# Performance work log

Measured on AMD Instinct MI355X. Metric: run time of the kernel, lower is better.

## Reference

```python
import jax, jax.numpy as jnp
from jax import lax
import numpy as np

B, N, T = 16, 1024, 12
H_DIM, D_FF, NHEADS = 64, 256, 4
SDIM, DDIM, WDIM = 32, 16, 15
D_IN = 1 + SDIM + DDIM + WDIM  # 64


def setup_inputs() -> dict:
    key = jax.random.key(0)
    ks = jax.random.split(key, 32)
    def p(k, shape, s=0.05):
        return jax.random.normal(k, shape, dtype=jnp.float32) * s
    h = H_DIM
    inp = {
        'flow': jax.random.normal(ks[0], (B, N, T), dtype=jnp.float32),
        'day_idx': jax.random.randint(ks[1], (B, N, T), 0, 288),
        'week_idx': jax.random.randint(ks[2], (B, N, T), 0, 7),
        'spatial_emb': p(ks[3], (N, SDIM)),
        'daily_emb': p(ks[4], (288, DDIM)),
        'weekly_emb': p(ks[5], (7, WDIM)),
        'gfs_fc_w': p(ks[6], (h, D_IN)), 'gfs_fc_b': jnp.zeros(h),
        'glu_w': p(ks[7], (2 * h, h)), 'glu_b': jnp.zeros(2 * h),
        'gc_weight': p(ks[8], (h, h)),
        'gc_A': p(ks[9], (N, N), 0.02), 'gc_A2': p(ks[10], (N, N), 0.02),
        'ds_init_w': p(ks[11], (2 * h, h, 1, 3)), 'ds_init_b': jnp.zeros(2 * h),
        'ds_p1m_w': p(ks[12], (h, h, 1, 3)), 'ds_p1m_b': jnp.zeros(h),
        'ds_p1g_w': p(ks[13], (h, h, 1, 3)), 'ds_p1g_b': jnp.zeros(h),
        'ds_p2m_w': p(ks[14], (h, h, 1, 3)), 'ds_p2m_b': jnp.zeros(h),
        'ds_p2g_w': p(ks[15], (h, h, 1, 3)), 'ds_p2g_b': jnp.zeros(h),
        'ds_fc_w': p(ks[16], (h, 2 * h)), 'ds_fc_b': jnp.zeros(h),
        'wq': p(ks[17], (h, h)), 'bq': jnp.zeros(h),
        'wk': p(ks[18], (h, h)), 'bk': jnp.zeros(h),
        'wv': p(ks[19], (h, h)), 'bv': jnp.zeros(h),
        'wo': p(ks[20], (h, h)), 'bo': jnp.zeros(h),
        'ff1_w': p(ks[21], (D_FF, h)), 'ff1_b': jnp.zeros(D_FF),
        'ff2_w': p(ks[22], (h, D_FF)), 'ff2_b': jnp.zeros(h),
        'ln1_g': jnp.ones(h), 'ln1_b': jnp.zeros(h),
        'ln2_g': jnp.ones(h), 'ln2_b': jnp.zeros(h),
        'cl_w': p(ks[23], (T,)), 'cl_b': jnp.zeros(()),
    }
    return inp


def _ln(x, g, b):
    m = jnp.mean(x, -1, keepdims=True)
    v = jnp.mean(jnp.square(x - m), -1, keepdims=True)
    return (x - m) * lax.rsqrt(v + 1e-5) * g + b


def _conv1xk(x, w, b):
    # x: [B, C, N, T], w: [O, I, 1, 3], padding (0,1) along time
    y = lax.conv_general_dilated(x, w, (1, 1), ((0, 0), (1, 1)),
                                 dimension_numbers=('NCHW', 'OIHW', 'NCHW'))
    return y + b[None, :, None, None]


def reference(flow, day_idx, week_idx, spatial_emb, daily_emb, weekly_emb,
              gfs_fc_w, gfs_fc_b, glu_w, glu_b, gc_weight, gc_A, gc_A2,
              ds_init_w, ds_init_b, ds_p1m_w, ds_p1m_b, ds_p1g_w, ds_p1g_b,
              ds_p2m_w, ds_p2m_b, ds_p2g_w, ds_p2g_b, ds_fc_w, ds_fc_b,
              wq, bq, wk, bk, wv, bv, wo, bo, ff1_w, ff1_b, ff2_w, ff2_b,
              ln1_g, ln1_b, ln2_g, ln2_b, cl_w, cl_b):
    h = H_DIM
    # --- InfoEmb: concat flow + spatial + daily + weekly embeddings ---
    sp = jnp.broadcast_to(spatial_emb[None, :, None, :], (B, N, T, SDIM))
    x = jnp.concatenate([flow[..., None], sp, daily_emb[day_idx], weekly_emb[week_idx]], -1)  # [B,N,T,64]
    # --- GFS: 1x1 conv + GLU (channels == last dim) ---
    x = x @ gfs_fc_w.T + gfs_fc_b
    g = x @ glu_w.T + glu_b
    lhs, rhs = g[..., :h], g[..., h:]
    x = lhs * jax.nn.sigmoid(rhs)  # [B,N,T,h]
    # --- TASTGC: adaptive spatial graph conv with two learned adjacencies ---
    A1 = jax.nn.softmax(jax.nn.relu(gc_A), axis=1)
    A2 = jax.nn.softmax(jax.nn.relu(gc_A2), axis=1)
    hs = jnp.einsum('mn,bntd->bmtd', A1, x) + jnp.einsum('mn,bntd->bmtd', A2, x)
    x = jax.nn.relu(jnp.einsum('bntd,de->bnte', hs, gc_weight))  # [B,N,T,h]
    # --- DSFIN: dual-path gated temporal conv ---
    xd = jnp.transpose(x, (0, 3, 1, 2))  # [B,h,N,T]
    x_init = _conv1xk(xd, ds_init_w, ds_init_b)  # [B,2h,N,T]
    p1, p2 = x_init[:, :h], x_init[:, h:]
    p1o = _conv1xk(p1, ds_p1m_w, ds_p1m_b) * jax.nn.sigmoid(_conv1xk(p1, ds_p1g_w, ds_p1g_b))
    p2o = _conv1xk(p2, ds_p2m_w, ds_p2m_b) * jax.nn.sigmoid(_conv1xk(p2, ds_p2g_w, ds_p2g_b))
    fused = jax.nn.relu(jnp.concatenate([p1o, p2o], 1) + x_init)  # [B,2h,N,T]
    fused = jnp.transpose(fused, (0, 2, 3, 1))  # [B,N,T,2h]
    x = fused @ ds_fc_w.T + ds_fc_b  # [B,N,T,h]
    # --- EncoderLayer: multi-head attention along time per node ---
    dk = h // NHEADS
    y = x.reshape(B * N, T, h)
    q = (y @ wq.T + bq).reshape(B * N, T, NHEADS, dk)
    k = (y @ wk.T + bk).reshape(B * N, T, NHEADS, dk)
    v = (y @ wv.T + bv).reshape(B * N, T, NHEADS, dk)
    scores = jnp.einsum('blhd,bshd->bhls', q, k) / jnp.sqrt(jnp.float32(dk))
    attn = jax.nn.softmax(scores, -1)
    o = jnp.einsum('bhls,bshd->blhd', attn, v).reshape(B * N, T, h)
    y1 = _ln(y + (o @ wo.T + bo), ln1_g, ln1_b)
    ff = jax.nn.relu(y1 @ ff1_w.T + ff1_b) @ ff2_w.T + ff2_b
    y2 = _ln(y1 + ff, ln2_g, ln2_b).reshape(B, N, T, h)
    # --- CongestionLearn: symmetric sigmoid node-node gate from flow ---
    f = jax.nn.relu(flow @ cl_w + cl_b)  # [B,N]
    m = jnp.mean(f, 0)  # [N]
    fuse = jax.nn.sigmoid((m[:, None] + m[None, :]) * 0.5)  # [N,N]
    out = jnp.einsum('mn,bntd->bmtd', fuse, y2)  # [B,N,T,h]
    return out
```

## Files before the change

kernel.cpp:

```cpp
#include <hip/hip_runtime.h>
#include <cstdint>

#define B_ 16
#define N_ 1024
#define T_ 12
#define HD 64
#define BN_ (B_*N_)
#define BNT (B_*N_*T_)
#define TD (T_*HD)

typedef __attribute__((ext_vector_type(8))) short short8;
typedef __attribute__((ext_vector_type(4))) float f32x4;

#define MFMA16(a,b,c) __builtin_amdgcn_mfma_f32_16x16x32_bf16(a,b,c,0,0,0)

__device__ __forceinline__ float sigmoidf_(float x) { return 1.f / (1.f + __expf(-x)); }

__device__ __forceinline__ unsigned short f2bf(float f) {
  unsigned int u = __float_as_uint(f);
  u += 0x7fffu + ((u >> 16) & 1u);
  return (unsigned short)(u >> 16);
}
__device__ __forceinline__ float bf2f(unsigned short h) {
  unsigned int u = ((unsigned int)h) << 16;
  return __uint_as_float(u);
}

#define F4E(v, ii) ((ii)==0?(v).x:((ii)==1?(v).y:((ii)==2?(v).z:(v).w)))

__device__ __forceinline__ float blkRedMax(float v, float* red) {
  #pragma unroll
  for (int off = 32; off >= 1; off >>= 1) v = fmaxf(v, __shfl_xor(v, off));
  int w = threadIdx.x >> 6;
  if ((threadIdx.x & 63) == 0) red[w] = v;
  __syncthreads();
  v = fmaxf(fmaxf(red[0], red[1]), fmaxf(red[2], red[3]));
  __syncthreads();
  return v;
}
__device__ __forceinline__ float blkRedSum(float v, float* red) {
  #pragma unroll
  for (int off = 32; off >= 1; off >>= 1) v += __shfl_xor(v, off);
  int w = threadIdx.x >> 6;
  if ((threadIdx.x & 63) == 0) red[w] = v;
  __syncthreads();
  v = red[0] + red[1] + red[2] + red[3];
  __syncthreads();
  return v;
}

__global__ void k_wprep_e(const float* __restrict__ w1, const float* __restrict__ w2,
                          float* __restrict__ wT)
{
  int tid = blockIdx.x*256 + threadIdx.x;
  if (tid < 4096) { int d = tid >> 6, j = tid & 63; wT[j*64 + d] = w1[tid]; }
  if (tid < 8192) { int o = tid >> 6, j = tid & 63; wT[4096 + j*128 + o] = w2[tid]; }
}

__global__ void k_wprep3(const float* __restrict__ wi,
                         const float* __restrict__ w1m, const float* __restrict__ w1g,
                         const float* __restrict__ w2m, const float* __restrict__ w2g,
                         const float* __restrict__ wfc, unsigned short* __restrict__ W)
{
  int t = blockIdx.x*256 + threadIdx.x;
  {
    int o = t / 192, k = t - o*192, tap = k >> 6, i = k & 63;
    W[o*192 + k] = f2bf(wi[(o*64 + i)*3 + tap]);
  }
  if (t < 12288) {
    int o = t / 192, k = t - o*192, tap = k >> 6, i = k & 63;
    int src = (o*64 + i)*3 + tap;
    W[24576 + o*192 + k]      = f2bf(w1m[src]);
    W[24576 + (64+o)*192 + k] = f2bf(w1g[src]);
    W[49152 + o*192 + k]      = f2bf(w2m[src]);
    W[49152 + (64+o)*192 + k] = f2bf(w2g[src]);
  }
  if (t < 8192) W[73728 + t] = f2bf(wfc[t]);
}

__global__ void k_wprep4(const float* __restrict__ wq, const float* __restrict__ wk,
                         const float* __restrict__ wv, const float* __restrict__ wo,
                         const float* __restrict__ f1w, const float* __restrict__ f2w,
                         unsigned short* __restrict__ W)
{
  int t = blockIdx.x*256 + threadIdx.x;
  if (t < 4096)        W[t] = f2bf(wq[t]);
  else if (t < 8192)   W[t] = f2bf(wk[t-4096]);
  else if (t < 12288)  W[t] = f2bf(wv[t-8192]);
  else if (t < 16384)  W[t] = f2bf(wo[t-12288]);
  else if (t < 32768)  W[t] = f2bf(f1w[t-16384]);
  else                 W[t] = f2bf(f2w[t-32768]);
}

__global__ __launch_bounds__(256) void k_embed2(
    const float* __restrict__ flow, const int* __restrict__ day, const int* __restrict__ week,
    const float* __restrict__ semb, const float* __restrict__ demb, const float* __restrict__ wemb,
    const float* __restrict__ wT, const float* __restrict__ b1,
    const float* __restrict__ b2, const float* __restrict__ gcw,
    unsigned short* __restrict__ outw)
{
  __shared__ float4 vb_all[4][256];
  int lane = threadIdx.x & 63, wid = threadIdx.x >> 6;
  float4* vb = vb_all[wid];
  const float* w1T = wT;
  const float* w2T = wT + 4096;
  int row0 = (blockIdx.x*4 + wid) * 16;

  float x[16];
  #pragma unroll
  for (int r = 0; r < 16; ++r) {
    int row = row0 + r;
    int n = (row / T_) & (N_-1);
    int c = lane;
    float val;
    if (c == 0)      val = flow[row];
    else if (c < 33) val = semb[n*32 + (c-1)];
    else if (c < 49) val = demb[day[row]*16 + (c-33)];
    else             val = wemb[week[row]*15 + (c-49)];
    x[r] = val;
  }
  #pragma unroll
  for (int q = 0; q < 4; ++q)
    vb[lane*4 + q] = make_float4(x[4*q], x[4*q+1], x[4*q+2], x[4*q+3]);

  float acc[16];
  {
    float bv = b1[lane];
    #pragma unroll
    for (int r = 0; r < 16; ++r) acc[r] = bv;
    for (int j = 0; j < 64; ++j) {
      float w = w1T[j*64 + lane];
      #pragma unroll
      for (int q = 0; q < 4; ++q) {
        float4 v = vb[j*4 + q];
        acc[4*q]   += w*v.x; acc[4*q+1] += w*v.y;
        acc[4*q+2] += w*v.z; acc[4*q+3] += w*v.w;
      }
    }
  }
  #pragma unroll
  for (int q = 0; q < 4; ++q)
    vb[lane*4 + q] = make_float4(acc[4*q], acc[4*q+1], acc[4*q+2], acc[4*q+3]);

  float lo[16], hi[16];
  {
    float blo = b2[lane], bhi = b2[64 + lane];
    #pragma unroll
    for (int r = 0; r < 16; ++r) { lo[r] = blo; hi[r] = bhi; }
    for (int j = 0; j < 64; ++j) {
      float wl = w2T[j*128 + lane];
      float wh = w2T[j*128 + 64 + lane];
      #pragma unroll
      for (int q = 0; q < 4; ++q) {
        float4 v = vb[j*4 + q];
        lo[4*q]   += wl*v.x; lo[4*q+1] += wl*v.y; lo[4*q+2] += wl*v.z; lo[4*q+3] += wl*v.w;
        hi[4*q]   += wh*v.x; hi[4*q+1] += wh*v.y; hi[4*q+2] += wh*v.z; hi[4*q+3] += wh*v.w;
      }
    }
    #pragma unroll
    for (int r = 0; r < 16; ++r) lo[r] = lo[r] * sigmoidf_(hi[r]);
  }
  #pragma unroll
  for (int q = 0; q < 4; ++q)
    vb[lane*4 + q] = make_float4(lo[4*q], lo[4*q+1], lo[4*q+2], lo[4*q+3]);

  {
    #pragma unroll
    for (int r = 0; r < 16; ++r) acc[r] = 0.f;
    for (int j = 0; j < 64; ++j) {
      float w = gcw[j*64 + lane];
      #pragma unroll
      for (int q = 0; q < 4; ++q) {
        float4 v = vb[j*4 + q];
        acc[4*q]   += w*v.x; acc[4*q+1] += w*v.y;
        acc[4*q+2] += w*v.z; acc[4*q+3] += w*v.w;
      }
    }
    #pragma unroll
    for (int r = 0; r < 16; ++r)
      outw[(size_t)(row0 + r)*64 + lane] = f2bf(acc[r]);
  }
}

__global__ __launch_bounds__(256) void k_aprep(
    const float* __restrict__ A1, const float* __restrict__ A2, unsigned short* __restrict__ Aout)
{
  __shared__ float red[4];
  int m = blockIdx.x, tid = threadIdx.x;
  float mx0, is0, mx1, is1;
  {
    const float* src = A1 + (size_t)m*N_;
    float mx = 0.f;
    for (int i = tid; i < N_; i += 256) mx = fmaxf(mx, fmaxf(src[i], 0.f));
    mx = blkRedMax(mx, red);
    float s = 0.f;
    for (int i = tid; i < N_; i += 256) s += __expf(fmaxf(src[i], 0.f) - mx);
    s = blkRedSum(s, red);
    mx0 = mx; is0 = 1.f / s;
  }
  {
    const float* src = A2 + (size_t)m*N_;
    float mx = 0.f;
    for (int i = tid; i < N_; i += 256) mx = fmaxf(mx, fmaxf(src[i], 0.f));
    mx = blkRedMax(mx, red);
    float s = 0.f;
    for (int i = tid; i < N_; i += 256) s += __expf(fmaxf(src[i], 0.f) - mx);
    s = blkRedSum(s, red);
    mx1 = mx; is1 = 1.f / s;
  }
  const float* s1 = A1 + (size_t)m*N_;
  const float* s2 = A2 + (size_t)m*N_;
  for (int i = tid; i < N_; i += 256) {
    float v1 = __expf(fmaxf(s1[i], 0.f) - mx0) * is0;
    float v2 = __expf(fmaxf(s2[i], 0.f) - mx1) * is1;
    Aout[(size_t)m*N_ + i] = f2bf(v1 + v2);
  }
}

template<int RELU, int OB16>
__global__ __launch_bounds__(256) void k_gemm_mfma(
    const unsigned short* __restrict__ A, const unsigned short* __restrict__ X,
    void* __restrict__ C, int K, int P)
{
  __shared__ unsigned short sA[128*40];
  __shared__ unsigned short sB[128*40];
  int tid = threadIdx.x, lane = tid & 63, wid = tid >> 6;
  int M = gridDim.y * 128;
  int b = blockIdx.z;
  const unsigned short* Xb = X + (size_t)b*K*P;
  int m0 = blockIdx.y*128, p0 = blockIdx.x*128;
  int wr = wid >> 1, wc = wid & 1;

  f32x4 acc[4][4] = {};

  for (int k0 = 0; k0 < K; k0 += 32) {
    #pragma unroll
    for (int pass = 0; pass < 2; ++pass) {
      int r = (tid >> 2) + 64*pass, kk = (tid & 3)*8;
      short8 v = *(const short8*)&A[(size_t)(m0+r)*K + k0 + kk];
      *(short8*)&sA[r*40 + kk] = v;
    }
    #pragma unroll
    for (int pass = 0; pass < 4; ++pass) {
      int p  = (tid & 63) + 64*(pass & 1);
      int k4 = (tid >> 6)*4 + 16*(pass >> 1);
      ushort4 h;
      h.x = Xb[(size_t)(k0+k4+0)*P + p0 + p];
      h.y = Xb[(size_t)(k0+k4+1)*P + p0 + p];
      h.z = Xb[(size_t)(k0+k4+2)*P + p0 + p];
      h.w = Xb[(size_t)(k0+k4+3)*P + p0 + p];
      *(ushort4*)&sB[p*40 + k4] = h;
    }
    __syncthreads();
    short8 af[4], bf[4];
    #pragma unroll
    for (int f = 0; f < 4; ++f) {
      af[f] = *(const short8*)&sA[(wr*64 + f*16 + (lane & 15))*40 + (lane >> 4)*8];
      bf[f] = *(const short8*)&sB[(wc*64 + f*16 + (lane & 15))*40 + (lane >> 4)*8];
    }
    #pragma unroll
    for (int fm = 0; fm < 4; ++fm)
      #pragma unroll
      for (int fn = 0; fn < 4; ++fn)
        acc[fm][fn] = MFMA16(af[fm], bf[fn], acc[fm][fn]);
    __syncthreads();
  }
  #pragma unroll
  for (int fm = 0; fm < 4; ++fm) {
    int row = m0 + wr*64 + fm*16 + (lane >> 4)*4;
    #pragma unroll
    for (int fn = 0; fn < 4; ++fn) {
      int col = p0 + wc*64 + fn*16 + (lane & 15);
      #pragma unroll
      for (int r = 0; r < 4; ++r) {
        float v = acc[fm][fn][r];
        if (RELU) v = fmaxf(v, 0.f);
        if (OB16) {
          unsigned short* Cb = (unsigned short*)C + (size_t)b*M*P;
          Cb[(size_t)(row + r)*P + col] = f2bf(v);
        } else {
          float* Cb = (float*)C + (size_t)b*M*P;
          Cb[(size_t)(row + r)*P + col] = v;
        }
      }
    }
  }
}

__global__ __launch_bounds__(256) void k_ds3(
    const unsigned short* xds,
    const unsigned short* __restrict__ Wall,
    const float* __restrict__ bi,
    const float* __restrict__ b1m, const float* __restrict__ b1g,
    const float* __restrict__ b2m, const float* __restrict__ b2g,
    const float* __restrict__ bfc,
    unsigned short* outg)
{
  __shared__ unsigned short smem[36352];
  unsigned short* X_lds  = smem;
  unsigned short* xi_lds = smem + 8064;
  unsigned short* fu_lds = smem + 23296;
  const unsigned short* WiB  = Wall;
  const unsigned short* Wg1B = Wall + 24576;
  const unsigned short* Wg2B = Wall + 49152;
  const unsigned short* WfB  = Wall + 73728;

  int tid = threadIdx.x, lane = tid & 63, wid = tid >> 6;
  int l15 = lane & 15, l4 = lane >> 4;
  int bn0 = blockIdx.x * 8;

  for (int i = tid; i < 8*2*72; i += 256) {
    int g = i / 144, r = i - g*144;
    int tp = (r < 72) ? 0 : 13, c = (r < 72) ? r : r - 72;
    X_lds[(g*14 + tp)*72 + c] = 0;
  }
  for (int i = tid; i < 8*2*136; i += 256) {
    int g = i / 272, r = i - g*272;
    int tp = (r < 136) ? 0 : 13, c = (r < 136) ? r : r - 136;
    xi_lds[(g*14 + tp)*136 + c] = 0;
  }
  for (int i = tid; i < 768; i += 256) {
    int g = i / 96, rem = i - g*96, t = rem >> 3, i8 = rem & 7;
    short8 v = *(const short8*)&xds[(size_t)(bn0+g)*768 + t*64 + i8*8];
    *(short8*)&X_lds[(g*14 + t + 1)*72 + i8*8] = v;
  }
  __syncthreads();

  int ga[6], ta[6];
  #pragma unroll
  for (int mt = 0; mt < 6; ++mt) {
    int r = mt*16 + l15;
    ga[mt] = r / 12; ta[mt] = r - ga[mt]*12;
  }

  {
    f32x4 acc1[6][2] = {};
    int nb = wid*2;
    #pragma unroll
    for (int ks = 0; ks < 6; ++ks) {
      int tap = ks >> 1, i0 = (ks & 1)*32;
      short8 af[6];
      #pragma unroll
      for (int mt = 0; mt < 6; ++mt)
        af[mt] = *(const short8*)&X_lds[(ga[mt]*14 + ta[mt] + tap)*72 + i0 + l4*8];
      short8 bf0 = *(const short8*)&WiB[(size_t)((nb  )*16 + l15)*192 + ks*32 + l4*8];
      short8 bf1 = *(const short8*)&WiB[(size_t)((nb+1)*16 + l15)*192 + ks*32 + l4*8];
      #pragma unroll
      for (int mt = 0; mt < 6; ++mt) {
        acc1[mt][0] = MFMA16(af[mt], bf0, acc1[mt][0]);
        acc1[mt][1] = MFMA16(af[mt], bf1, acc1[mt][1]);
      }
    }
    #pragma unroll
    for (int nn = 0; nn < 2; ++nn) {
      int o = (nb+nn)*16 + l15;
      float bv = bi[o];
      #pragma unroll
      for (int mt = 0; mt < 6; ++mt) {
        #pragma unroll
        for (int reg = 0; reg < 4; ++reg) {
          int r = mt*16 + l4*4 + reg;
          int g = r / 12, t = r - g*12;
          xi_lds[(g*14 + t + 1)*136 + o] = f2bf(acc1[mt][nn][reg] + bv);
        }
      }
    }
  }
  __syncthreads();

  #pragma unroll
  for (int h = 0; h < 2; ++h) {
    const unsigned short* Wg = h ? Wg2B : Wg1B;
    f32x4 am[6] = {}, ag[6] = {};
    #pragma unroll
    for (int ks = 0; ks < 6; ++ks) {
      int tap = ks >> 1, i0 = (ks & 1)*32;
      short8 af[6];
      #pragma unroll
      for (int mt = 0; mt < 6; ++mt)
        af[mt] = *(const short8*)&xi_lds[(ga[mt]*14 + ta[mt] + tap)*136 + h*64 + i0 + l4*8];
      short8 bm = *(const short8*)&Wg[(size_t)(wid*16 + l15)*192 + ks*32 + l4*8];
      short8 bg = *(const short8*)&Wg[(size_t)((wid+4)*16 + l15)*192 + ks*32 + l4*8];
      #pragma unroll
      for (int mt = 0; mt < 6; ++mt) {
        am[mt] = MFMA16(af[mt], bm, am[mt]);
        ag[mt] = MFMA16(af[mt], bg, ag[mt]);
      }
    }
    int o = wid*16 + l15;
    float bmv = (h ? b2m : b1m)[o];
    float bgv = (h ? b2g : b1g)[o];
    #pragma unroll
    for (int mt = 0; mt < 6; ++mt) {
      #pragma unroll
      for (int reg = 0; reg < 4; ++reg) {
        int r = mt*16 + l4*4 + reg;
        int g = r / 12, t = r - g*12;
        float pm = am[mt][reg] + bmv;
        float pg = ag[mt][reg] + bgv;
        float po = pm * sigmoidf_(pg);
        float xi = bf2f(xi_lds[(g*14 + t + 1)*136 + h*64 + o]);
        fu_lds[r*136 + h*64 + o] = f2bf(fmaxf(po + xi, 0.f));
      }
    }
  }
  __syncthreads();

  {
    f32x4 a3[6] = {};
    #pragma unroll
    for (int ks = 0; ks < 4; ++ks) {
      short8 af = *(const short8*)&WfB[(size_t)(wid*16 + l15)*128 + ks*32 + l4*8];
      #pragma unroll
      for (int nt = 0; nt < 6; ++nt) {
        short8 bf = *(const short8*)&fu_lds[(nt*16 + l15)*136 + ks*32 + l4*8];
        a3[nt] = MFMA16(af, bf, a3[nt]);
      }
    }
    int e0 = wid*16 + l4*4;
    float4 bb = *(const float4*)&bfc[e0];
    #pragma unroll
    for (int nt = 0; nt < 6; ++nt) {
      ushort4 vv;
      vv.x = f2bf(a3[nt][0] + bb.x); vv.y = f2bf(a3[nt][1] + bb.y);
      vv.z = f2bf(a3[nt][2] + bb.z); vv.w = f2bf(a3[nt][3] + bb.w);
      *(ushort4*)&outg[((size_t)(bn0 + ga[nt])*12 + ta[nt])*64 + e0] = vv;
    }
  }
}

__global__ __launch_bounds__(256) void k_attn3(
    const unsigned short* __restrict__ xg,
    const unsigned short* __restrict__ Wat,
    const float* __restrict__ bq, const float* __restrict__ bk, const float* __restrict__ bv,
    const float* __restrict__ bo,
    const float* __restrict__ f1b, const float* __restrict__ f2b,
    const float* __restrict__ g1, const float* __restrict__ be1,
    const float* __restrict__ g2, const float* __restrict__ be2,
    unsigned short* __restrict__ outg)
{
  __shared__ unsigned short su[18432];
  __shared__ float part[2][4][48];
  __shared__ float stats[2][48];
  unsigned short* Ybuf = su;
  unsigned short* Qkv  = su + 3456;
  unsigned short* Hb   = su + 3456;
  unsigned short* atts = su + 16896;

  const unsigned short* Wqkv = Wat;
  const unsigned short* Wo   = Wat + 12288;
  const unsigned short* F1   = Wat + 16384;
  const unsigned short* F2   = Wat + 32768;

  int tid = threadIdx.x, lane = tid & 63, w = tid >> 6;
  int l15 = lane & 15, l4 = lane >> 4;
  size_t base = (size_t)blockIdx.x * 4 * 768;

  for (int i = tid; i < 384; i += 256) {
    int r = i >> 3, c = i & 7;
    *(short8*)&Ybuf[r*72 + c*8] = *(const short8*)&xg[base + r*64 + c*8];
  }
  __syncthreads();

  {
    f32x4 acc[3][3] = {};
    #pragma unroll
    for (int ks = 0; ks < 2; ++ks) {
      short8 af[3];
      #pragma unroll
      for (int mt = 0; mt < 3; ++mt)
        af[mt] = *(const short8*)&Ybuf[(mt*16 + l15)*72 + ks*32 + l4*8];
      #pragma unroll
      for (int i = 0; i < 3; ++i) {
        int nt = w*3 + i;
        short8 bf = *(const short8*)&Wqkv[(size_t)(nt*16 + l15)*64 + ks*32 + l4*8];
        #pragma unroll
        for (int mt = 0; mt < 3; ++mt)
          acc[mt][i] = MFMA16(af[mt], bf, acc[mt][i]);
      }
    }
    #pragma unroll
    for (int i = 0; i < 3; ++i) {
      int col = (w*3+i)*16 + l15;
      float bias = col < 64 ? bq[col] : (col < 128 ? bk[col-64] : bv[col-128]);
      #pragma unroll
      for (int mt = 0; mt < 3; ++mt)
        #pragma unroll
        for (int r = 0; r < 4; ++r)
          Qkv[(mt*16 + l4*4 + r)*216 + col] = f2bf(acc[mt][i][r] + bias);
    }
  }
  __syncthreads();

  {
    int rb = w*12;
    unsigned short* as = atts + w*384;
    #pragma unroll
    for (int h = 0; h < 4; ++h) {
      short8 kf = {}, qf = {};
      if (l4 < 2) {
        kf = *(const short8*)&Qkv[(rb + l15)*216 + 64 + h*16 + l4*8];
        qf = *(const short8*)&Qkv[(rb + l15)*216 +      h*16 + l4*8];
      }
      f32x4 sc = {};
      sc = MFMA16(kf, qf, sc);
      float e[4]; float mx = -3e38f;
      #pragma unroll
      for (int r = 0; r < 4; ++r) {
        float v = (l4 == 3) ? -3e38f : sc[r]*0.25f;
        e[r] = v; mx = fmaxf(mx, v);
      }
      mx = fmaxf(mx, __shfl_xor(mx, 16));
      mx = fmaxf(mx, __shfl_xor(mx, 32));
      float s = 0.f;
      #pragma unroll
      for (int r = 0; r < 4; ++r) { e[r] = __expf(e[r] - mx); s += e[r]; }
      s += __shfl_xor(s, 16); s += __shfl_xor(s, 32);
      float inv = 1.f/s;
      ushort4 pk;
      pk.x = f2bf(e[0]*inv); pk.y = f2bf(e[1]*inv);
      pk.z = f2bf(e[2]*inv); pk.w = f2bf(e[3]*inv);
      *(ushort4*)&as[l15*24 + l4*4] = pk;
      short8 aaf = {};
      if (l4 < 2) aaf = *(const short8*)&as[l15*24 + l4*8];
      short8 vf = {};
      if (l4 < 2) {
        #pragma unroll
        for (int j = 0; j < 8; ++j) {
          int s_ = l4*8 + j;
          vf[j] = (s_ < 12) ? (short)Qkv[(rb + s_)*216 + 128 + h*16 + l15] : (short)0;
        }
      }
      f32x4 o = {};
      o = MFMA16(aaf, vf, o);
      if (l4 < 3) {
        #pragma unroll
        for (int r = 0; r < 4; ++r)
          Ybuf[(rb + l4*4 + r)*72 + h*16 + l15] = f2bf(o[r]);
      }
    }
  }
  __syncthreads();

  {
    f32x4 zacc[3] = {};
    #pragma unroll
    for (int ks = 0; ks < 2; ++ks) {
      short8 bf = *(const short8*)&Wo[(size_t)(w*16 + l15)*64 + ks*32 + l4*8];
      #pragma unroll
      for (int mt = 0; mt < 3; ++mt) {
        short8 af = *(const short8*)&Ybuf[(mt*16 + l15)*72 + ks*32 + l4*8];
        zacc[mt] = MFMA16(af, bf, zacc[mt]);
      }
    }
    int col = w*16 + l15;
    float bias = bo[col];
    #pragma unroll
    for (int mt = 0; mt < 3; ++mt)
      #pragma unroll
      for (int r = 0; r < 4; ++r) {
        int row = mt*16 + l4*4 + r;
        float z = zacc[mt][r] + bias + bf2f(xg[base + row*64 + col]);
        zacc[mt][r] = z;
        float s1 = z, s2 = z*z;
        #pragma unroll
        for (int off = 1; off <= 8; off <<= 1) { s1 += __shfl_xor(s1, off); s2 += __shfl_xor(s2, off); }
        if (l15 == 0) { part[0][w][row] = s1; part[1][w][row] = s2; }
      }
    __syncthreads();
    if (tid < 48) {
      float s = part[0][0][tid]+part[0][1][tid]+part[0][2][tid]+part[0][3][tid];
      float q = part[1][0][tid]+part[1][1][tid]+part[1][2][tid]+part[1][3][tid];
      float mu = s * (1.f/64.f);
      float var = q * (1.f/64.f) - mu*mu;
      stats[0][tid] = mu; stats[1][tid] = rsqrtf(var + 1e-5f);
    }
    __syncthreads();
    float gv = g1[col], bvv = be1[col];
    #pragma unroll
    for (int mt = 0; mt < 3; ++mt)
      #pragma unroll
      for (int r = 0; r < 4; ++r) {
        int row = mt*16 + l4*4 + r;
        Ybuf[row*72 + col] = f2bf((zacc[mt][r] - stats[0][row]) * stats[1][row] * gv + bvv);
      }
  }
  __syncthreads();

  {
    f32x4 acc[3][4] = {};
    #pragma unroll
    for (int ks = 0; ks < 2; ++ks) {
      short8 af[3];
      #pragma unroll
      for (int mt = 0; mt < 3; ++mt)
        af[mt] = *(const short8*)&Ybuf[(mt*16 + l15)*72 + ks*32 + l4*8];
      #pragma unroll
      for (int i = 0; i < 4; ++i) {
        int nt = w*4 + i;
        short8 bf = *(const short8*)&F1[(size_t)(nt*16 + l15)*64 + ks*32 + l4*8];
        #pragma unroll
        for (int mt = 0; mt < 3; ++mt)
          acc[mt][i] = MFMA16(af[mt], bf, acc[mt][i]);
      }
    }
    #pragma unroll
    for (int i = 0; i < 4; ++i) {
      int col = (w*4+i)*16 + l15;
      float bias = f1b[col];
      #pragma unroll
      for (int mt = 0; mt < 3; ++mt)
        #pragma unroll
        for (int r = 0; r < 4; ++r)
          Hb[(mt*16 + l4*4 + r)*280 + col] = f2bf(fmaxf(acc[mt][i][r] + bias, 0.f));
    }
  }
  __syncthreads();

  {
    f32x4 acc[3] = {};
    #pragma unroll
    for (int ks = 0; ks < 8; ++ks) {
      short8 bf = *(const short8*)&F2[(size_t)(w*16 + l15)*256 + ks*32 + l4*8];
      #pragma unroll
      for (int mt = 0; mt < 3; ++mt) {
        short8 af = *(const short8*)&Hb[(mt*16 + l15)*280 + ks*32 + l4*8];
        acc[mt] = MFMA16(af, bf, acc[mt]);
      }
    }
    int col = w*16 + l15;
    float bias = f2b[col];
    #pragma unroll
    for (int mt = 0; mt < 3; ++mt)
      #pragma unroll
      for (int r = 0; r < 4; ++r) {
        int row = mt*16 + l4*4 + r;
        float z = acc[mt][r] + bias + bf2f(Ybuf[row*72 + col]);
        acc[mt][r] = z;
        float s1 = z, s2 = z*z;
        #pragma unroll
        for (int off = 1; off <= 8; off <<= 1) { s1 += __shfl_xor(s1, off); s2 += __shfl_xor(s2, off); }
        if (l15 == 0) { part[0][w][row] = s1; part[1][w][row] = s2; }
      }
    __syncthreads();
    if (tid < 48) {
      float s = part[0][0][tid]+part[0][1][tid]+part[0][2][tid]+part[0][3][tid];
      float q = part[1][0][tid]+part[1][1][tid]+part[1][2][tid]+part[1][3][tid];
      float mu = s * (1.f/64.f);
      float var = q * (1.f/64.f) - mu*mu;
      stats[0][tid] = mu; stats[1][tid] = rsqrtf(var + 1e-5f);
    }
    __syncthreads();
    float gv = g2[col], bvv = be2[col];
    #pragma unroll
    for (int mt = 0; mt < 3; ++mt)
      #pragma unroll
      for (int r = 0; r < 4; ++r) {
        int row = mt*16 + l4*4 + r;
        outg[base + row*64 + col] = f2bf((acc[mt][r] - stats[0][row]) * stats[1][row] * gv + bvv);
      }
  }
}

__global__ void k_mvec(const float* __restrict__ flow, const float* __restrict__ clw,
                       const float* __restrict__ clb, float* __restrict__ mv)
{
  int n = blockIdx.x*blockDim.x + threadIdx.x;
  if (n < N_) {
    float s = 0.f;
    float bias = clb[0];
    for (int b = 0; b < B_; ++b) {
      const float* f = flow + ((size_t)b*N_ + n)*T_;
      float acc = bias;
      #pragma unroll
      for (int t = 0; t < T_; ++t) acc += f[t]*clw[t];
      s += fmaxf(acc, 0.f);
    }
    mv[n] = s * (1.f/16.f);
  }
}

__global__ void k_fusemat(const float* __restrict__ mv, unsigned short* __restrict__ F)
{
  int idx = blockIdx.x*256 + threadIdx.x;
  int m = idx >> 10, n = idx & 1023;
  float x = 0.5f*(mv[m] + mv[n]);
  F[idx] = f2bf(1.f/(1.f + __expf(-x)));
}

extern "C" void kernel_launch(void* const* d_in, const int* in_sizes, int n_in,
                              void* d_out, int out_size, void* d_ws, size_t ws_size,
                              hipStream_t stream)
{
  const float* flow = (const float*)d_in[0];
  const int*   day  = (const int*)d_in[1];
  const int*   week = (const int*)d_in[2];
  const float* semb = (const float*)d_in[3];
  const float* demb = (const float*)d_in[4];
  const float* wemb = (const float*)d_in[5];
  const float* gfsw = (const float*)d_in[6];
  const float* gfsb = (const float*)d_in[7];
  const float* gluw = (const float*)d_in[8];
  const float* glub = (const float*)d_in[9];
  const float* gcw  = (const float*)d_in[10];
  const float* gcA  = (const float*)d_in[11];
  const float* gcA2 = (const float*)d_in[12];
  const float* wi   = (const float*)d_in[13];
  const float* bi   = (const float*)d_in[14];
  const float* w1m  = (const float*)d_in[15];
  const float* b1m  = (const float*)d_in[16];
  const float* w1g  = (const float*)d_in[17];
  const float* b1g  = (const float*)d_in[18];
  const float* w2m  = (const float*)d_in[19];
  const float* b2m  = (const float*)d_in[20];
  const float* w2g  = (const float*)d_in[21];
  const float* b2g  = (const float*)d_in[22];
  const float* wfc  = (const float*)d_in[23];
  const float* bfc  = (const float*)d_in[24];
  const float* wq   = (const float*)d_in[25];
  const float* bq   = (const float*)d_in[26];
  const float* wk   = (const float*)d_in[27];
  const float* bk   = (const float*)d_in[28];
  const float* wv   = (const float*)d_in[29];
  const float* bv   = (const float*)d_in[30];
  const float* wo   = (const float*)d_in[31];
  const float* bo   = (const float*)d_in[32];
  const float* f1w  = (const float*)d_in[33];
  const float* f1b  = (const float*)d_in[34];
  const float* f2w  = (const float*)d_in[35];
  const float* f2b  = (const float*)d_in[36];
  const float* g1   = (const float*)d_in[37];
  const float* be1  = (const float*)d_in[38];
  const float* g2   = (const float*)d_in[39];
  const float* be2  = (const float*)d_in[40];
  const float* clw  = (const float*)d_in[41];
  const float* clb  = (const float*)d_in[42];

  float* out = (float*)d_out;
  char* ws = (char*)d_ws;
  unsigned short* Amat = (unsigned short*)ws;
  float* mv  = (float*)(ws + (size_t)2*1024*1024);
  float* wTe = (float*)(ws + (size_t)2*1024*1024 + 64*1024);
  unsigned short* wds = (unsigned short*)(ws + (size_t)2*1024*1024 + 128*1024);
  unsigned short* wat = (unsigned short*)(ws + (size_t)2*1024*1024 + 320*1024);
  unsigned short* xw  = (unsigned short*)(ws + (size_t)3*1024*1024);
  unsigned short* xds = (unsigned short*)(ws + (size_t)28*1024*1024);

  k_wprep_e<<<48, 256, 0, stream>>>(gfsw, gluw, wTe);
  k_wprep3<<<96, 256, 0, stream>>>(wi, w1m, w1g, w2m, w2g, wfc, wds);
  k_wprep4<<<192, 256, 0, stream>>>(wq, wk, wv, wo, f1w, f2w, wat);
  k_embed2<<<BNT/64, 256, 0, stream>>>(flow, day, week, semb, demb, wemb,
                                       wTe, gfsb, glub, gcw, xw);
  k_aprep<<<N_, 256, 0, stream>>>(gcA, gcA2, Amat);
  dim3 gg(TD/128, N_/128, B_);
  k_gemm_mfma<1,1><<<gg, 256, 0, stream>>>(Amat, xw, xds, N_, TD);
  k_ds3<<<BN_/8, 256, 0, stream>>>(xds, wds, bi, b1m, b1g, b2m, b2g, bfc, xds);
  k_attn3<<<BN_/4, 256, 0, stream>>>(xds, wat, bq, bk, bv, bo, f1b, f2b,
                                     g1, be1, g2, be2, xw);
  k_mvec<<<N_/256, 256, 0, stream>>>(flow, clw, clb, mv);
  k_fusemat<<<(N_*N_)/256, 256, 0, stream>>>(mv, Amat);
  k_gemm_mfma<0,0><<<gg, 256, 0, stream>>>(Amat, xw, out, N_, TD);
}
```

Before: 386.6 us.

## Rewrite embedding MLP chain with bf16 MFMA tiles in shared memory

The fused embed kernel (input linear, GLU, graph-conv weight) moves from scalar fp32 FMAs per lane to bf16 16x16x32 MFMA instructions. Each block now handles 128 rows staged in padded shared-memory tiles. The weight prep kernel emits bf16 weights, including a transposed copy of the graph-conv weight. This trades fp32 accuracy in the embedding path for bf16 rounding of intermediates, in exchange for matrix-core throughput.

```diff
diff --git a/kernel.cpp b/kernel.cpp
--- a/kernel.cpp
+++ b/kernel.cpp
@@ -26,8 +26,6 @@
   return __uint_as_float(u);
 }
 
-#define F4E(v, ii) ((ii)==0?(v).x:((ii)==1?(v).y:((ii)==2?(v).z:(v).w)))
-
 __device__ __forceinline__ float blkRedMax(float v, float* red) {
   #pragma unroll
   for (int off = 32; off >= 1; off >>= 1) v = fmaxf(v, __shfl_xor(v, off));
@@ -49,12 +47,16 @@
   return v;
 }
 
-__global__ void k_wprep_e(const float* __restrict__ w1, const float* __restrict__ w2,
-                          float* __restrict__ wT)
-{
-  int tid = blockIdx.x*256 + threadIdx.x;
-  if (tid < 4096) { int d = tid >> 6, j = tid & 63; wT[j*64 + d] = w1[tid]; }
-  if (tid < 8192) { int o = tid >> 6, j = tid & 63; wT[4096 + j*128 + o] = w2[tid]; }
+__global__ void k_wprep_e2(const float* __restrict__ w1, const float* __restrict__ w2,
+                           const float* __restrict__ gcw, unsigned short* __restrict__ W)
+{
+  int t = blockIdx.x*256 + threadIdx.x;
+  if (t < 4096)       W[t] = f2bf(w1[t]);
+  else if (t < 12288) W[t] = f2bf(w2[t-4096]);
+  else {
+    int r = t - 12288, e = r >> 6, d = r & 63;
+    W[12288 + e*64 + d] = f2bf(gcw[d*64 + e]);
+  }
 }
 
 __global__ void k_wprep3(const float* __restrict__ wi,
@@ -92,93 +94,96 @@
   else                 W[t] = f2bf(f2w[t-32768]);
 }
 
-__global__ __launch_bounds__(256) void k_embed2(
+__global__ __launch_bounds__(256) void k_embed3(
     const float* __restrict__ flow, const int* __restrict__ day, const int* __restrict__ week,
     const float* __restrict__ semb, const float* __restrict__ demb, const float* __restrict__ wemb,
-    const float* __restrict__ wT, const float* __restrict__ b1,
-    const float* __restrict__ b2, const float* __restrict__ gcw,
+    const unsigned short* __restrict__ wTe, const float* __restrict__ b1,
+    const float* __restrict__ b2,
     unsigned short* __restrict__ outw)
 {
-  __shared__ float4 vb_all[4][256];
-  int lane = threadIdx.x & 63, wid = threadIdx.x >> 6;
-  float4* vb = vb_all[wid];
-  const float* w1T = wT;
-  const float* w2T = wT + 4096;
-  int row0 = (blockIdx.x*4 + wid) * 16;
-
-  float x[16];
-  #pragma unroll
-  for (int r = 0; r < 16; ++r) {
+  __shared__ unsigned short sEa[128*72];
+  __shared__ unsigned short sEb[128*72];
+  const unsigned short* W1  = wTe;
+  const unsigned short* W2  = wTe + 4096;
+  const unsigned short* GcT = wTe + 12288;
+
+  int tid = threadIdx.x, lane = tid & 63, w = tid >> 6;
+  int l15 = lane & 15, l4 = lane >> 4;
+  int row0 = blockIdx.x * 128;
+
+  for (int i = tid; i < 8192; i += 256) {
+    int r = i >> 6, c = i & 63;
     int row = row0 + r;
     int n = (row / T_) & (N_-1);
-    int c = lane;
     float val;
     if (c == 0)      val = flow[row];
     else if (c < 33) val = semb[n*32 + (c-1)];
     else if (c < 49) val = demb[day[row]*16 + (c-33)];
     else             val = wemb[week[row]*15 + (c-49)];
-    x[r] = val;
-  }
-  #pragma unroll
-  for (int q = 0; q < 4; ++q)
-    vb[lane*4 + q] = make_float4(x[4*q], x[4*q+1], x[4*q+2], x[4*q+3]);
-
-  float acc[16];
-  {
-    float bv = b1[lane];
-    #pragma unroll
-    for (int r = 0; r < 16; ++r) acc[r] = bv;
-    for (int j = 0; j < 64; ++j) {
-      float w = w1T[j*64 + lane];
-      #pragma unroll
-      for (int q = 0; q < 4; ++q) {
-        float4 v = vb[j*4 + q];
-        acc[4*q]   += w*v.x; acc[4*q+1] += w*v.y;
-        acc[4*q+2] += w*v.z; acc[4*q+3] += w*v.w;
-      }
-    }
-  }
-  #pragma unroll
-  for (int q = 0; q < 4; ++q)
-    vb[lane*4 + q] = make_float4(acc[4*q], acc[4*q+1], acc[4*q+2], acc[4*q+3]);
-
-  float lo[16], hi[16];
-  {
-    float blo = b2[lane], bhi = b2[64 + lane];
-    #pragma unroll
-    for (int r = 0; r < 16; ++r) { lo[r] = blo; hi[r] = bhi; }
-    for (int j = 0; j < 64; ++j) {
-      float wl = w2T[j*128 + lane];
-      float wh = w2T[j*128 + 64 + lane];
-      #pragma unroll
-      for (int q = 0; q < 4; ++q) {
-        float4 v = vb[j*4 + q];
-        lo[4*q]   += wl*v.x; lo[4*q+1] += wl*v.y; lo[4*q+2] += wl*v.z; lo[4*q+3] += wl*v.w;
-        hi[4*q]   += wh*v.x; hi[4*q+1] += wh*v.y; hi[4*q+2] += wh*v.z; hi[4*q+3] += wh*v.w;
-      }
-    }
-    #pragma unroll
-    for (int r = 0; r < 16; ++r) lo[r] = lo[r] * sigmoidf_(hi[r]);
-  }
-  #pragma unroll
-  for (int q = 0; q < 4; ++q)
-    vb[lane*4 + q] = make_float4(lo[4*q], lo[4*q+1], lo[4*q+2], lo[4*q+3]);
-
-  {
-    #pragma unroll
-    for (int r = 0; r < 16; ++r) acc[r] = 0.f;
-    for (int j = 0; j < 64; ++j) {
-      float w = gcw[j*64 + lane];
-      #pragma unroll
-      for (int q = 0; q < 4; ++q) {
-        float4 v = vb[j*4 + q];
-        acc[4*q]   += w*v.x; acc[4*q+1] += w*v.y;
-        acc[4*q+2] += w*v.z; acc[4*q+3] += w*v.w;
-      }
-    }
-    #pragma unroll
-    for (int r = 0; r < 16; ++r)
-      outw[(size_t)(row0 + r)*64 + lane] = f2bf(acc[r]);
+    sEa[r*72 + c] = f2bf(val);
+  }
+  __syncthreads();
+
+  {
+    f32x4 acc[8] = {};
+    #pragma unroll
+    for (int ks = 0; ks < 2; ++ks) {
+      short8 bf = *(const short8*)&W1[(w*16 + l15)*64 + ks*32 + l4*8];
+      #pragma unroll
+      for (int mt = 0; mt < 8; ++mt) {
+        short8 af = *(const short8*)&sEa[(mt*16 + l15)*72 + ks*32 + l4*8];
+        acc[mt] = MFMA16(af, bf, acc[mt]);
+      }
+    }
+    float bias = b1[w*16 + l15];
+    #pragma unroll
+    for (int mt = 0; mt < 8; ++mt)
+      #pragma unroll
+      for (int r = 0; r < 4; ++r)
+        sEb[(mt*16 + l4*4 + r)*72 + w*16 + l15] = f2bf(acc[mt][r] + bias);
+  }
+  __syncthreads();
+
+  {
+    f32x4 alo[8] = {}, ahi[8] = {};
+    #pragma unroll
+    for (int ks = 0; ks < 2; ++ks) {
+      short8 blo = *(const short8*)&W2[(size_t)(w*16 + l15)*64 + ks*32 + l4*8];
+      short8 bhi = *(const short8*)&W2[(size_t)(64 + w*16 + l15)*64 + ks*32 + l4*8];
+      #pragma unroll
+      for (int mt = 0; mt < 8; ++mt) {
+        short8 af = *(const short8*)&sEb[(mt*16 + l15)*72 + ks*32 + l4*8];
+        alo[mt] = MFMA16(af, blo, alo[mt]);
+        ahi[mt] = MFMA16(af, bhi, ahi[mt]);
+      }
+    }
+    float blov = b2[w*16 + l15], bhiv = b2[64 + w*16 + l15];
+    #pragma unroll
+    for (int mt = 0; mt < 8; ++mt)
+      #pragma unroll
+      for (int r = 0; r < 4; ++r) {
+        float v = (alo[mt][r] + blov) * sigmoidf_(ahi[mt][r] + bhiv);
+        sEa[(mt*16 + l4*4 + r)*72 + w*16 + l15] = f2bf(v);
+      }
+  }
+  __syncthreads();
+
+  {
+    f32x4 acc[8] = {};
+    #pragma unroll
+    for (int ks = 0; ks < 2; ++ks) {
+      short8 bf = *(const short8*)&GcT[(w*16 + l15)*64 + ks*32 + l4*8];
+      #pragma unroll
+      for (int mt = 0; mt < 8; ++mt) {
+        short8 af = *(const short8*)&sEa[(mt*16 + l15)*72 + ks*32 + l4*8];
+        acc[mt] = MFMA16(af, bf, acc[mt]);
+      }
+    }
+    #pragma unroll
+    for (int mt = 0; mt < 8; ++mt)
+      #pragma unroll
+      for (int r = 0; r < 4; ++r)
+        outw[(size_t)(row0 + mt*16 + l4*4 + r)*64 + w*16 + l15] = f2bf(acc[mt][r]);
   }
 }
 
@@ -740,17 +745,17 @@
   char* ws = (char*)d_ws;
   unsigned short* Amat = (unsigned short*)ws;
   float* mv  = (float*)(ws + (size_t)2*1024*1024);
-  float* wTe = (float*)(ws + (size_t)2*1024*1024 + 64*1024);
+  unsigned short* wTe = (unsigned short*)(ws + (size_t)2*1024*1024 + 64*1024);
   unsigned short* wds = (unsigned short*)(ws + (size_t)2*1024*1024 + 128*1024);
   unsigned short* wat = (unsigned short*)(ws + (size_t)2*1024*1024 + 320*1024);
   unsigned short* xw  = (unsigned short*)(ws + (size_t)3*1024*1024);
   unsigned short* xds = (unsigned short*)(ws + (size_t)28*1024*1024);
 
-  k_wprep_e<<<48, 256, 0, stream>>>(gfsw, gluw, wTe);
+  k_wprep_e2<<<64, 256, 0, stream>>>(gfsw, gluw, gcw, wTe);
   k_wprep3<<<96, 256, 0, stream>>>(wi, w1m, w1g, w2m, w2g, wfc, wds);
   k_wprep4<<<192, 256, 0, stream>>>(wq, wk, wv, wo, f1w, f2w, wat);
-  k_embed2<<<BNT/64, 256, 0, stream>>>(flow, day, week, semb, demb, wemb,
-                                       wTe, gfsb, glub, gcw, xw);
+  k_embed3<<<BNT/128, 256, 0, stream>>>(flow, day, week, semb, demb, wemb,
+                                        wTe, gfsb, glub, xw);
   k_aprep<<<N_, 256, 0, stream>>>(gcA, gcA2, Amat);
   dim3 gg(TD/128, N_/128, B_);
   k_gemm_mfma<1,1><<<gg, 256, 0, stream>>>(Amat, xw, xds, N_, TD);
```

After: 341.2 us. -11.7%, faster.
